# Kernel optimization log

Measured on AMD Instinct MI355X. Metric: run time of the kernel, lower is better.

Reference implementation:

```python
import jax, jax.numpy as jnp
import numpy as np


def setup_inputs() -> dict:
    key = jax.random.key(0)
    k1, k2, k3, k4, k5 = jax.random.split(key, 5)
    x = jax.random.normal(k1, (32, 256, 56, 56), dtype=jnp.float32)
    q_weight = jax.random.randint(k2, (256, 256, 3, 3), 0, 256, dtype=jnp.int32)
    w_scale = jax.random.uniform(k3, (), dtype=jnp.float32) * 0.01 + 1e-4
    w_min = -jax.random.uniform(k4, (), dtype=jnp.float32)
    bias = jax.random.normal(k5, (256,), dtype=jnp.float32)
    return {"x": x, "q_weight": q_weight, "w_scale": w_scale, "w_min": w_min, "bias": bias}


def reference(x, q_weight, w_scale, w_min, bias):
    # Dequantize: affine min/scale scheme -> w = q * scale + min
    w = q_weight.astype(jnp.float32) * w_scale + w_min  # [O, I, kh, kw]
    out = jax.lax.conv_general_dilated(
        x, w,
        window_strides=(1, 1),
        padding=((1, 1), (1, 1)),
        lhs_dilation=(1, 1),
        rhs_dilation=(1, 1),  # dilation=1
        dimension_numbers=("NCHW", "OIHW", "NCHW"),
        feature_group_count=1,  # groups=1
    )
    return out + bias[None, :, None, None]
```

## Files before the change

### kernel.cpp

```cpp
#include <hip/hip_runtime.h>
#include <hip/hip_bf16.h>


typedef __bf16 bf16x8 __attribute__((ext_vector_type(8)));
typedef float floatx4 __attribute__((ext_vector_type(4)));

#define XT_ELEMS 25690112L

__global__ void dequant_w(const int* __restrict__ q, const float* __restrict__ sp,
                          const float* __restrict__ mp, __hip_bfloat16* __restrict__ w2) {
  int idx = blockIdx.x * 256 + threadIdx.x;
  float s = sp[0], m = mp[0];
  int i = idx & 255;
  int o = (idx >> 8) & 255;
  int k9 = idx >> 16;
  float w = (float)q[(o * 256 + i) * 9 + k9] * s + m;
  w2[idx] = __float2bfloat16(w);
}

__global__ void transpose_x(const float* __restrict__ x, __hip_bfloat16* __restrict__ xt) {
  __shared__ float tile[64][68];
  int n = blockIdx.z;
  int cb = blockIdx.y << 6;
  int pb = blockIdx.x << 6;
  int t = threadIdx.x;

  const float* src = x + ((long)(n * 256 + cb)) * 3136 + pb;
#pragma unroll
  for (int it = 0; it < 4; it++) {
    int flat = it * 1024 + t * 4;
    int c = flat >> 6, p = flat & 63;
    float4 v = *(const float4*)(src + (long)c * 3136 + p);
    *(float4*)&tile[c][p] = v;
  }
  __syncthreads();
  __hip_bfloat16* dst = xt + ((long)(n * 3136 + pb)) * 256 + cb;
#pragma unroll
  for (int it = 0; it < 4; it++) {
    int flat = it * 1024 + t * 4;
    int p = flat >> 6, c = flat & 63;
    union {
      ushort4 u;
      __hip_bfloat16 h[4];
    } tmp;
#pragma unroll
    for (int j = 0; j < 4; j++) tmp.h[j] = __float2bfloat16(tile[c + j][p]);
    *(ushort4*)(dst + (long)p * 256 + c) = tmp.u;
  }
}

__global__ __launch_bounds__(256, 2) void conv_mfma(
    const __hip_bfloat16* __restrict__ xt, const __hip_bfloat16* __restrict__ w2,
    const float* __restrict__ bias, float* __restrict__ out) {
  __shared__ __align__(16) __hip_bfloat16 xs[6 * 58 * 40];
  __shared__ __align__(16) __hip_bfloat16 wsh[128 * 40];

  int ob = blockIdx.x;
  int rb = blockIdx.y;
  int n = blockIdx.z;
  int t = threadIdx.x;
  int lane = t & 63;
  int wid = t >> 6;
  int wo = (wid & 1) << 6;
  int wpx = (wid >> 1) * 112;
  int l15 = lane & 15, quad = lane >> 4;
  int o0 = ob << 7;
  int h0 = rb << 2;

  int baddr[7];
#pragma unroll
  for (int tt = 0; tt < 7; tt++) {
    int px = wpx + tt * 16 + l15;
    int r = px / 56, c = px - r * 56;
    baddr[tt] = (r * 58 + c) * 40 + quad * 8;
  }

  int xlds[6];
  int xgo[6];
#pragma unroll
  for (int it = 0; it < 6; it++) {
    int q = t + it * 256;
    xlds[it] = -1;
    xgo[it] = -1;
    if (q < 1392) {
      int pos = q >> 2, ck = q & 3;
      int row = pos / 58, col = pos - row * 58;
      int h = h0 - 1 + row, w = col - 1;
      bool v = (h >= 0) && (h < 56) && (w >= 0) && (w < 56);
      xlds[it] = pos * 40 + ck * 8;
      if (v) xgo[it] = (n * 3136 + h * 56 + w) * 256 + ck * 8;
    }
  }

  floatx4 acc[4][7];
#pragma unroll
  for (int m = 0; m < 4; m++)
#pragma unroll
    for (int tt = 0; tt < 7; tt++) acc[m][tt] = (floatx4){0.f, 0.f, 0.f, 0.f};

  for (int ib = 0; ib < 8; ib++) {
    int i0 = ib * 32;
    for (int k9 = 0; k9 < 9; k9++) {
      if (k9 == 0) {
#pragma unroll
        for (int it = 0; it < 6; it++) {
          if (xlds[it] >= 0) {
            int4 v = {0, 0, 0, 0};
            if (xgo[it] >= 0) v = *(const int4*)((const void*)(xt + xgo[it] + i0));
            *(int4*)((void*)(xs + xlds[it])) = v;
          }
        }
      }
      {
        int base = (k9 * 256 + o0) * 256 + i0;
#pragma unroll
        for (int it = 0; it < 2; it++) {
          int q2 = t + it * 256;
          int o_r = q2 >> 2, ck = q2 & 3;
          int4 v = *(const int4*)((const void*)(w2 + base + o_r * 256 + ck * 8));
          *(int4*)((void*)(wsh + o_r * 40 + ck * 8)) = v;
        }
      }
      __syncthreads();

      int kh = k9 / 3, kw = k9 - kh * 3;
      int koff = (kh * 58 + kw) * 40;
      bf16x8 a[4];
#pragma unroll
      for (int m = 0; m < 4; m++)
        a[m] = *(const bf16x8*)((const void*)(wsh + (wo + m * 16 + l15) * 40 + quad * 8));
#pragma unroll
      for (int tt = 0; tt < 7; tt++) {
        bf16x8 b = *(const bf16x8*)((const void*)(xs + baddr[tt] + koff));
#pragma unroll
        for (int m = 0; m < 4; m++)
          acc[m][tt] = __builtin_amdgcn_mfma_f32_16x16x32_bf16(a[m], b, acc[m][tt], 0, 0, 0);
      }
      __syncthreads();
    }
  }

#pragma unroll
  for (int m = 0; m < 4; m++) {
    int obase = o0 + wo + m * 16 + quad * 4;
#pragma unroll
    for (int r = 0; r < 4; r++) {
      int o = obase + r;
      float bv = bias[o];
      int outb = (n * 256 + o) * 3136 + h0 * 56;
#pragma unroll
      for (int tt = 0; tt < 7; tt++) {
        int px = wpx + tt * 16 + l15;
        out[outb + px] = acc[m][tt][r] + bv;
      }
    }
  }
}

extern "C" void kernel_launch(void* const* d_in, const int* in_sizes, int n_in,
                              void* d_out, int out_size, void* d_ws, size_t ws_size,
                              hipStream_t stream) {
  const float* x = (const float*)d_in[0];
  const int* qw = (const int*)d_in[1];
  const float* wscale = (const float*)d_in[2];
  const float* wmin = (const float*)d_in[3];
  const float* bias = (const float*)d_in[4];
  float* out = (float*)d_out;

  __hip_bfloat16* xt = (__hip_bfloat16*)d_ws;
  __hip_bfloat16* w2 = (__hip_bfloat16*)((char*)d_ws + XT_ELEMS * 2);

  dequant_w<<<2304, 256, 0, stream>>>(qw, wscale, wmin, w2);
  transpose_x<<<dim3(49, 4, 32), 256, 0, stream>>>(x, xt);
  conv_mfma<<<dim3(2, 14, 32), 256, 0, stream>>>(xt, w2, bias, out);
}
```

Before: 318.9 us.

## Stage three weight taps per barrier pair, drop LDS transpose, vectorize dequant reads

The conv kernel now loads the weights for all three kw taps of a kernel row into a tripled LDS buffer, cutting barrier pairs per channel block from nine to three. Halo zero-fill moves out of the loop because padded positions never change. transpose_x drops its shared-memory tile and has each thread transpose a 4x4 register block with strided reads. dequant_w has each thread read nine contiguous ints and write them strided. The costs are more LDS per block, which may hurt occupancy, and less coalesced global access in the transpose and dequant kernels.

```diff
diff --git a/kernel.cpp b/kernel.cpp
--- a/kernel.cpp
+++ b/kernel.cpp
@@ -9,43 +9,44 @@
 
 __global__ void dequant_w(const int* __restrict__ q, const float* __restrict__ sp,
                           const float* __restrict__ mp, __hip_bfloat16* __restrict__ w2) {
-  int idx = blockIdx.x * 256 + threadIdx.x;
+  int g = blockIdx.x * 256 + threadIdx.x;
   float s = sp[0], m = mp[0];
-  int i = idx & 255;
-  int o = (idx >> 8) & 255;
-  int k9 = idx >> 16;
-  float w = (float)q[(o * 256 + i) * 9 + k9] * s + m;
-  w2[idx] = __float2bfloat16(w);
+  const int* qp = q + (long)g * 9;
+#pragma unroll
+  for (int j = 0; j < 9; j++) {
+    float w = (float)qp[j] * s + m;
+    w2[(long)j * 65536 + g] = __float2bfloat16(w);
+  }
 }
 
-__global__ void transpose_x(const float* __restrict__ x, __hip_bfloat16* __restrict__ xt) {
-  __shared__ float tile[64][68];
-  int n = blockIdx.z;
-  int cb = blockIdx.y << 6;
+__global__ __launch_bounds__(256) void transpose_x(const float* __restrict__ x,
+                                                   __hip_bfloat16* __restrict__ xt) {
+  int n = blockIdx.y;
   int pb = blockIdx.x << 6;
   int t = threadIdx.x;
+  int c0 = (t & 63) << 2;
+  int p0 = (t >> 6) << 4;
 
-  const float* src = x + ((long)(n * 256 + cb)) * 3136 + pb;
+  const float* src = x + (long)n * 802816 + pb;
+  __hip_bfloat16* dst = xt + ((long)(n * 3136 + pb)) * 256;
+
 #pragma unroll
-  for (int it = 0; it < 4; it++) {
-    int flat = it * 1024 + t * 4;
-    int c = flat >> 6, p = flat & 63;
-    float4 v = *(const float4*)(src + (long)c * 3136 + p);
-    *(float4*)&tile[c][p] = v;
-  }
-  __syncthreads();
-  __hip_bfloat16* dst = xt + ((long)(n * 3136 + pb)) * 256 + cb;
+  for (int pi = 0; pi < 4; pi++) {
+    int p = p0 + pi * 4;
+    float v[4][4];
 #pragma unroll
-  for (int it = 0; it < 4; it++) {
-    int flat = it * 1024 + t * 4;
-    int p = flat >> 6, c = flat & 63;
-    union {
-      ushort4 u;
-      __hip_bfloat16 h[4];
-    } tmp;
+    for (int cj = 0; cj < 4; cj++)
+      *(float4*)v[cj] = *(const float4*)(src + (long)(c0 + cj) * 3136 + p);
 #pragma unroll
-    for (int j = 0; j < 4; j++) tmp.h[j] = __float2bfloat16(tile[c + j][p]);
-    *(ushort4*)(dst + (long)p * 256 + c) = tmp.u;
+    for (int j = 0; j < 4; j++) {
+      union {
+        ushort4 u;
+        __hip_bfloat16 h[4];
+      } r;
+#pragma unroll
+      for (int cj = 0; cj < 4; cj++) r.h[cj] = __float2bfloat16(v[cj][j]);
+      *(ushort4*)(dst + (long)(p + j) * 256 + c0) = r.u;
+    }
   }
 }
 
@@ -53,7 +54,7 @@
     const __hip_bfloat16* __restrict__ xt, const __hip_bfloat16* __restrict__ w2,
     const float* __restrict__ bias, float* __restrict__ out) {
   __shared__ __align__(16) __hip_bfloat16 xs[6 * 58 * 40];
-  __shared__ __align__(16) __hip_bfloat16 wsh[128 * 40];
+  __shared__ __align__(16) __hip_bfloat16 wsh[3 * 128 * 40];
 
   int ob = blockIdx.x;
   int rb = blockIdx.y;
@@ -92,6 +93,10 @@
     }
   }
 
+#pragma unroll
+  for (int it = 0; it < 6; it++)
+    if (xlds[it] >= 0 && xgo[it] < 0) *(int4*)((void*)(xs + xlds[it])) = (int4){0, 0, 0, 0};
+
   floatx4 acc[4][7];
 #pragma unroll
   for (int m = 0; m < 4; m++)
@@ -100,43 +105,41 @@
 
   for (int ib = 0; ib < 8; ib++) {
     int i0 = ib * 32;
-    for (int k9 = 0; k9 < 9; k9++) {
-      if (k9 == 0) {
+    for (int kh = 0; kh < 3; kh++) {
+      __syncthreads();
+      if (kh == 0) {
 #pragma unroll
-        for (int it = 0; it < 6; it++) {
-          if (xlds[it] >= 0) {
-            int4 v = {0, 0, 0, 0};
-            if (xgo[it] >= 0) v = *(const int4*)((const void*)(xt + xgo[it] + i0));
-            *(int4*)((void*)(xs + xlds[it])) = v;
-          }
-        }
+        for (int it = 0; it < 6; it++)
+          if (xgo[it] >= 0)
+            *(int4*)((void*)(xs + xlds[it])) = *(const int4*)((const void*)(xt + xgo[it] + i0));
       }
-      {
-        int base = (k9 * 256 + o0) * 256 + i0;
 #pragma unroll
-        for (int it = 0; it < 2; it++) {
-          int q2 = t + it * 256;
-          int o_r = q2 >> 2, ck = q2 & 3;
-          int4 v = *(const int4*)((const void*)(w2 + base + o_r * 256 + ck * 8));
-          *(int4*)((void*)(wsh + o_r * 40 + ck * 8)) = v;
-        }
+      for (int it = 0; it < 6; it++) {
+        int q2 = t + it * 256;
+        int tap = q2 >> 9;
+        int rem = q2 & 511;
+        int o_r = rem >> 2, ck = rem & 3;
+        int4 v = *(const int4*)((const void*)(
+            w2 + ((long)(kh * 3 + tap) * 256 + o0 + o_r) * 256 + i0 + ck * 8));
+        *(int4*)((void*)(wsh + (tap * 128 + o_r) * 40 + ck * 8)) = v;
       }
       __syncthreads();
 
-      int kh = k9 / 3, kw = k9 - kh * 3;
-      int koff = (kh * 58 + kw) * 40;
-      bf16x8 a[4];
 #pragma unroll
-      for (int m = 0; m < 4; m++)
-        a[m] = *(const bf16x8*)((const void*)(wsh + (wo + m * 16 + l15) * 40 + quad * 8));
-#pragma unroll
-      for (int tt = 0; tt < 7; tt++) {
-        bf16x8 b = *(const bf16x8*)((const void*)(xs + baddr[tt] + koff));
+      for (int kw = 0; kw < 3; kw++) {
+        int koff = (kh * 58 + kw) * 40;
+        bf16x8 a[4];
 #pragma unroll
         for (int m = 0; m < 4; m++)
-          acc[m][tt] = __builtin_amdgcn_mfma_f32_16x16x32_bf16(a[m], b, acc[m][tt], 0, 0, 0);
+          a[m] = *(const bf16x8*)((const void*)(wsh + (kw * 128 + wo + m * 16 + l15) * 40 + quad * 8));
+#pragma unroll
+        for (int tt = 0; tt < 7; tt++) {
+          bf16x8 b = *(const bf16x8*)((const void*)(xs + baddr[tt] + koff));
+#pragma unroll
+          for (int m = 0; m < 4; m++)
+            acc[m][tt] = __builtin_amdgcn_mfma_f32_16x16x32_bf16(a[m], b, acc[m][tt], 0, 0, 0);
+        }
       }
-      __syncthreads();
     }
   }
 
@@ -170,7 +173,7 @@
   __hip_bfloat16* xt = (__hip_bfloat16*)d_ws;
   __hip_bfloat16* w2 = (__hip_bfloat16*)((char*)d_ws + XT_ELEMS * 2);
 
-  dequant_w<<<2304, 256, 0, stream>>>(qw, wscale, wmin, w2);
-  transpose_x<<<dim3(49, 4, 32), 256, 0, stream>>>(x, xt);
+  dequant_w<<<256, 256, 0, stream>>>(qw, wscale, wmin, w2);
+  transpose_x<<<dim3(49, 32), 256, 0, stream>>>(x, xt);
   conv_mfma<<<dim3(2, 14, 32), 256, 0, stream>>>(xt, w2, bias, out);
 }
```

Result: no change. 318.2 us (-0.2%).
